# Kernel tuning notes

Measured on AMD Instinct MI355X. Metric: run time of the kernel, lower is better.

## Reference

```python
import jax, jax.numpy as jnp
import numpy as np

TWO_PI = 2.0 * np.pi
EPS = 1e-6

def collect_neighbors(h, edge_idx):
    # h: (B, L, D), edge_idx: (B, L, K) -> (B, L, K, D)
    B, L, K = edge_idx.shape
    D = h.shape[-1]
    flat = jnp.take_along_axis(h, edge_idx.reshape(B, L * K)[..., None], axis=1)
    return flat.reshape(B, L, K, D)

def normalize(v):
    return v / (jnp.linalg.norm(v, axis=-1, keepdims=True) + EPS)

def frames_inverse(X, C):
    # Gram-Schmidt backbone frames: R (B,L,3,3) columns [e1,e2,e3], t = CA
    N, CA, Cc = X[..., 0, :], X[..., 1, :], X[..., 2, :]
    e1 = normalize(N - CA)
    u2 = normalize(Cc - CA)
    e2 = normalize(u2 - jnp.sum(u2 * e1, axis=-1, keepdims=True) * e1)
    e3 = jnp.cross(e1, e2)
    R = jnp.stack([e1, e2, e3], axis=-1)  # (B,L,3,3)
    mask = (C > 0).astype(X.dtype)[..., None]  # (B,L,1)
    t = mask * CA
    R = mask[..., None] * R
    return R, t

def fourier(x, W):
    # x: (..., d_in), W: (d_in, dim_embedding//2)
    h = TWO_PI * jnp.einsum('...d,de->...e', x, W)
    return jnp.concatenate([jnp.cos(h), jnp.sin(h)], axis=-1)

def setup_inputs() -> dict:
    key = jax.random.key(0)
    k1, k2, k3, k4 = jax.random.split(key, 4)
    B, L, K, A = 2, 4096, 32, 4
    half = 128  # dim_embedding // 2
    X = jax.random.normal(k1, (B, L, A, 3), dtype=jnp.float32)
    edge_idx = jax.random.randint(k2, (B, L, K), 0, L)
    C = jnp.ones((B, L), dtype=jnp.int64)
    W_vec = jax.random.normal(k3, (3, half), dtype=jnp.float32)
    W_dist = jax.random.normal(k4, (64, half), dtype=jnp.float32)
    return {"X": X, "edge_idx": edge_idx, "C": C, "W_vec": W_vec, "W_dist": W_dist}

def reference(X, edge_idx, C, W_vec, W_dist):
    B, L, K = edge_idx.shape
    A = X.shape[2]
    # --- Edge2grids: concat i and neighbor-j 1mer coordinates ---
    X_flat = X.reshape(B, L, A * 3)
    X_j = collect_neighbors(X_flat, edge_idx)                      # (B,L,K,A*3)
    X_i = jnp.broadcast_to(X_flat[:, :, None, :], X_j.shape)
    X_ij = jnp.concatenate([X_i, X_j], axis=-1).reshape(B, L, K, 2 * A, 3)
    # --- pairwise distances among the 2A atoms -> (B,L,K,(2A)^2) ---
    dX = X_ij[..., :, None, :] - X_ij[..., None, :, :]
    D_ij = jnp.sqrt(jnp.sum(dX * dX, axis=-1) + EPS)
    D_ij = D_ij.reshape(B, L, K, (2 * A) * (2 * A))                # (B,L,K,64)
    # --- rigid frames + inner-transform composition ---
    R_i, t_i = frames_inverse(X, C)                                # (B,L,3,3), (B,L,3)
    R_j = collect_neighbors(R_i.reshape(B, L, 9), edge_idx).reshape(B, L, K, 3, 3)
    t_j = collect_neighbors(t_i, edge_idx)                         # (B,L,K,3)
    # R_ji = R_i^T R_j ; t_ji = R_i^T (t_j - t_i)
    t_ji = jnp.einsum('blmn,blkm->blkn', R_i, t_j - t_i[:, :, None, :])
    # --- random Fourier features ---
    edge_h = fourier(t_ji, W_vec) + fourier(D_ij, W_dist)          # (B,L,K,256)
    return edge_h
```

## Files before the change

kernel.cpp:

```cpp
#include <hip/hip_runtime.h>


namespace {

constexpr int Bb   = 2;
constexpr int Ll   = 4096;
constexpr int Kk   = 32;
constexpr int HALF = 128;
constexpr float FEPS = 1e-6f;

__device__ __forceinline__ float bcast(float x, int srclane) {
    return __int_as_float(__builtin_amdgcn_readlane(__float_as_int(x), srclane));
}

__global__ __launch_bounds__(128) void edge_rff(
    const float* __restrict__ X,
    const int*   __restrict__ edge_idx,
    const float* __restrict__ Wv,
    const float* __restrict__ Wd,
    float* __restrict__ out)
{
    const int bl   = blockIdx.x;
    const int b    = bl >> 12;
    const int e    = threadIdx.x;
    const int lane = threadIdx.x & 63;

    float w[22];
#pragma unroll
    for (int p = 0; p < 4; ++p)
#pragma unroll
        for (int q = 0; q < 4; ++q)
            w[p*4+q] = Wd[(p*8 + (q+4))*HALF + e] + Wd[((q+4)*8 + p)*HALF + e];

    constexpr int PJ[6] = {0,0,0,1,1,2};
    constexpr int QJ[6] = {1,2,3,2,3,3};
#pragma unroll
    for (int t = 0; t < 6; ++t)
        w[16+t] = Wd[((PJ[t]+4)*8 + (QJ[t]+4))*HALF + e]
                + Wd[((QJ[t]+4)*8 + (PJ[t]+4))*HALF + e];

    float wii[6];
#pragma unroll
    for (int t = 0; t < 6; ++t)
        wii[t] = Wd[(PJ[t]*8 + QJ[t])*HALF + e] + Wd[(QJ[t]*8 + PJ[t])*HALF + e];

    float wdiag = 0.0f;
#pragma unroll
    for (int p = 0; p < 8; ++p) wdiag += Wd[(p*8 + p)*HALF + e];

    const float wv0 = Wv[e], wv1 = Wv[HALF + e], wv2 = Wv[2*HALF + e];

    const float* Xi = X + (size_t)bl * 12;
    const float ai[4][3] = {
        {Xi[0], Xi[1], Xi[2]},
        {Xi[3], Xi[4], Xi[5]},
        {Xi[6], Xi[7], Xi[8]},
        {Xi[9], Xi[10], Xi[11]}
    };

    float cdot = 1.0e-3f * wdiag;
#pragma unroll
    for (int t = 0; t < 6; ++t) {
        const float dx = ai[PJ[t]][0] - ai[QJ[t]][0];
        const float dy = ai[PJ[t]][1] - ai[QJ[t]][1];
        const float dz = ai[PJ[t]][2] - ai[QJ[t]][2];
        cdot = fmaf(sqrtf(fmaf(dx,dx,fmaf(dy,dy,fmaf(dz,dz,FEPS)))), wii[t], cdot);
    }

    const float CAx = ai[1][0], CAy = ai[1][1], CAz = ai[1][2];
    const float v1x = ai[0][0]-CAx, v1y = ai[0][1]-CAy, v1z = ai[0][2]-CAz;
    const float inv1 = 1.0f/(sqrtf(v1x*v1x+v1y*v1y+v1z*v1z)+FEPS);
    const float e1x=v1x*inv1, e1y=v1y*inv1, e1z=v1z*inv1;
    const float v2x = ai[2][0]-CAx, v2y = ai[2][1]-CAy, v2z = ai[2][2]-CAz;
    const float inv2 = 1.0f/(sqrtf(v2x*v2x+v2y*v2y+v2z*v2z)+FEPS);
    const float u2x=v2x*inv2, u2y=v2y*inv2, u2z=v2z*inv2;
    const float dp = u2x*e1x+u2y*e1y+u2z*e1z;
    const float w2x=u2x-dp*e1x, w2y=u2y-dp*e1y, w2z=u2z-dp*e1z;
    const float inv3 = 1.0f/(sqrtf(w2x*w2x+w2y*w2y+w2z*w2z)+FEPS);
    const float e2x=w2x*inv3, e2y=w2y*inv3, e2z=w2z*inv3;
    const float e3x=e1y*e2z-e1z*e2y;
    const float e3y=e1z*e2x-e1x*e2z;
    const float e3z=e1x*e2y-e1y*e2x;

    int pA, pB;
    bool afromj;
    if (lane < 16)      { afromj = false; pA = lane >> 2; pB = lane & 3; }
    else if (lane < 22) { const int tt = lane - 16; afromj = true;
                          pA = (tt < 3) ? 0 : ((tt < 5) ? 1 : 2);
                          pB = (tt < 3) ? (tt + 1) : ((tt < 5) ? (tt - 1) : 3); }
    else                { afromj = false; pA = 0; pB = 0; }
    const float* paConst = Xi + pA * 3;
    const int aoff = pA * 3, boff = pB * 3;

    const int* eidx = edge_idx + (size_t)bl * Kk;
    const int cbase = b * Ll;

    for (int k = 0; k < Kk; ++k) {
        const int j = eidx[k];
        const float* Xj = X + (size_t)(cbase + j) * 12;

        const float* pa = afromj ? (Xj + aoff) : paConst;
        const float* pb = Xj + boff;
        const float dx = pa[0]-pb[0], dy = pa[1]-pb[1], dz = pa[2]-pb[2];
        const float Dlane = sqrtf(fmaf(dx,dx,fmaf(dy,dy,fmaf(dz,dz,FEPS))));

        const float ux = Xj[3]-CAx, uy = Xj[4]-CAy, uz = Xj[5]-CAz;
        const float t0 = e1x*ux + e1y*uy + e1z*uz;
        const float t1 = e2x*ux + e2y*uy + e2z*uz;
        const float t2 = e3x*ux + e3y*uy + e3z*uz;

        float a0 = cdot, a1 = 0.0f, a2 = 0.0f, a3 = 0.0f;
#pragma unroll
        for (int tt = 0; tt < 20; tt += 4) {
            a0 = fmaf(bcast(Dlane, tt+0), w[tt+0], a0);
            a1 = fmaf(bcast(Dlane, tt+1), w[tt+1], a1);
            a2 = fmaf(bcast(Dlane, tt+2), w[tt+2], a2);
            a3 = fmaf(bcast(Dlane, tt+3), w[tt+3], a3);
        }
        a0 = fmaf(bcast(Dlane, 20), w[20], a0);
        a1 = fmaf(bcast(Dlane, 21), w[21], a1);
        const float r2 = (a0 + a1) + (a2 + a3);
        const float r1 = fmaf(t0, wv0, fmaf(t1, wv1, t2 * wv2));

        const float f1 = __builtin_amdgcn_fractf(r1);
        const float f2 = __builtin_amdgcn_fractf(r2);
        const float s1 = __builtin_amdgcn_sinf(f1);
        const float c1 = __builtin_amdgcn_cosf(f1);
        const float s2 = __builtin_amdgcn_sinf(f2);
        const float c2 = __builtin_amdgcn_cosf(f2);

        float* o = out + ((size_t)(bl * Kk + k)) * 256;
        __builtin_nontemporal_store(c1 + c2, o + e);
        __builtin_nontemporal_store(s1 + s2, o + e + 128);
    }
}

}

extern "C" void kernel_launch(void* const* d_in, const int* in_sizes, int n_in,
                              void* d_out, int out_size, void* d_ws, size_t ws_size,
                              hipStream_t stream) {
    const float* X  = (const float*)d_in[0];
    const int*   ei = (const int*)d_in[1];
    const float* Wv = (const float*)d_in[3];
    const float* Wd = (const float*)d_in[4];
    float*       o  = (float*)d_out;

    dim3 grid(Bb * Ll);
    dim3 block(128);
    hipLaunchKernelGGL(edge_rff, grid, block, 0, stream, X, ei, Wv, Wd, o);
}
```

Measured before the change: 326.9 us.

## Precompute per-edge distances and rotated offsets into LDS before the output loop

The kernel now computes all 22 pairwise distances and the three rotated translation components for all 32 neighbours up front. The work is spread across the block's threads and staged in a shared-memory table, followed by one barrier. The output loop then reads these values with vector LDS loads instead of issuing a serial gather and readlane broadcasts per neighbour. This removes the dependent global-load latency and the scalar broadcast chain from each loop iteration, at the cost of LDS traffic, a __syncthreads, and some idle threads in the staging phase.

```diff
diff --git a/kernel.cpp b/kernel.cpp
--- a/kernel.cpp
+++ b/kernel.cpp
@@ -9,10 +9,6 @@
 constexpr int HALF = 128;
 constexpr float FEPS = 1e-6f;
 
-__device__ __forceinline__ float bcast(float x, int srclane) {
-    return __int_as_float(__builtin_amdgcn_readlane(__float_as_int(x), srclane));
-}
-
 __global__ __launch_bounds__(128) void edge_rff(
     const float* __restrict__ X,
     const int*   __restrict__ edge_idx,
@@ -20,10 +16,11 @@
     const float* __restrict__ Wd,
     float* __restrict__ out)
 {
-    const int bl   = blockIdx.x;
-    const int b    = bl >> 12;
-    const int e    = threadIdx.x;
-    const int lane = threadIdx.x & 63;
+    const int bl = blockIdx.x;
+    const int b  = bl >> 12;
+    const int e  = threadIdx.x;
+
+    __shared__ float ed[Kk][28];
 
     float w[22];
 #pragma unroll
@@ -51,27 +48,30 @@
     const float wv0 = Wv[e], wv1 = Wv[HALF + e], wv2 = Wv[2*HALF + e];
 
     const float* Xi = X + (size_t)bl * 12;
-    const float ai[4][3] = {
-        {Xi[0], Xi[1], Xi[2]},
-        {Xi[3], Xi[4], Xi[5]},
-        {Xi[6], Xi[7], Xi[8]},
-        {Xi[9], Xi[10], Xi[11]}
-    };
+    const float Nx  = Xi[0], Ny  = Xi[1], Nz  = Xi[2];
+    const float CAx = Xi[3], CAy = Xi[4], CAz = Xi[5];
+    const float Ccx = Xi[6], Ccy = Xi[7], Ccz = Xi[8];
+    const float Ox  = Xi[9], Oy  = Xi[10], Oz = Xi[11];
 
     float cdot = 1.0e-3f * wdiag;
+    {
+        const float px[4] = {Nx, CAx, Ccx, Ox};
+        const float py[4] = {Ny, CAy, Ccy, Oy};
+        const float pz[4] = {Nz, CAz, Ccz, Oz};
 #pragma unroll
-    for (int t = 0; t < 6; ++t) {
-        const float dx = ai[PJ[t]][0] - ai[QJ[t]][0];
-        const float dy = ai[PJ[t]][1] - ai[QJ[t]][1];
-        const float dz = ai[PJ[t]][2] - ai[QJ[t]][2];
-        cdot = fmaf(sqrtf(fmaf(dx,dx,fmaf(dy,dy,fmaf(dz,dz,FEPS)))), wii[t], cdot);
+        for (int t = 0; t < 6; ++t) {
+            const float dx = px[PJ[t]] - px[QJ[t]];
+            const float dy = py[PJ[t]] - py[QJ[t]];
+            const float dz = pz[PJ[t]] - pz[QJ[t]];
+            cdot = fmaf(sqrtf(fmaf(dx,dx,fmaf(dy,dy,fmaf(dz,dz,FEPS)))),
+                        wii[t], cdot);
+        }
     }
 
-    const float CAx = ai[1][0], CAy = ai[1][1], CAz = ai[1][2];
-    const float v1x = ai[0][0]-CAx, v1y = ai[0][1]-CAy, v1z = ai[0][2]-CAz;
+    const float v1x = Nx-CAx, v1y = Ny-CAy, v1z = Nz-CAz;
     const float inv1 = 1.0f/(sqrtf(v1x*v1x+v1y*v1y+v1z*v1z)+FEPS);
     const float e1x=v1x*inv1, e1y=v1y*inv1, e1z=v1z*inv1;
-    const float v2x = ai[2][0]-CAx, v2y = ai[2][1]-CAy, v2z = ai[2][2]-CAz;
+    const float v2x = Ccx-CAx, v2y = Ccy-CAy, v2z = Ccz-CAz;
     const float inv2 = 1.0f/(sqrtf(v2x*v2x+v2y*v2y+v2z*v2z)+FEPS);
     const float u2x=v2x*inv2, u2y=v2y*inv2, u2z=v2z*inv2;
     const float dp = u2x*e1x+u2y*e1y+u2z*e1z;
@@ -82,45 +82,68 @@
     const float e3y=e1z*e2x-e1x*e2z;
     const float e3z=e1x*e2y-e1y*e2x;
 
-    int pA, pB;
-    bool afromj;
-    if (lane < 16)      { afromj = false; pA = lane >> 2; pB = lane & 3; }
-    else if (lane < 22) { const int tt = lane - 16; afromj = true;
-                          pA = (tt < 3) ? 0 : ((tt < 5) ? 1 : 2);
-                          pB = (tt < 3) ? (tt + 1) : ((tt < 5) ? (tt - 1) : 3); }
-    else                { afromj = false; pA = 0; pB = 0; }
-    const float* paConst = Xi + pA * 3;
-    const int aoff = pA * 3, boff = pB * 3;
+    const int* eidx  = edge_idx + (size_t)bl * Kk;
+    const int  cbase = b * Ll;
 
-    const int* eidx = edge_idx + (size_t)bl * Kk;
-    const int cbase = b * Ll;
-
-    for (int k = 0; k < Kk; ++k) {
-        const int j = eidx[k];
+#pragma unroll
+    for (int i = 0; i < 8; ++i) {
+        const int id   = threadIdx.x + i * 128;
+        const int edge = id >> 5;
+        const int slot = id & 31;
+        if (slot >= 25) continue;
+        const int j = eidx[edge];
         const float* Xj = X + (size_t)(cbase + j) * 12;
 
-        const float* pa = afromj ? (Xj + aoff) : paConst;
-        const float* pb = Xj + boff;
-        const float dx = pa[0]-pb[0], dy = pa[1]-pb[1], dz = pa[2]-pb[2];
-        const float Dlane = sqrtf(fmaf(dx,dx,fmaf(dy,dy,fmaf(dz,dz,FEPS))));
+        float val;
+        if (slot < 22) {
+            const int tt  = (slot >= 16) ? (slot - 16) : 0;
+            const int pja = (0x211000 >> (4*tt)) & 0xF;
+            const int qja = (0x332321 >> (4*tt)) & 0xF;
+            const float* pa = (slot < 16) ? (Xi + (slot >> 2) * 3)
+                                          : (Xj + pja * 3);
+            const float* pb = (slot < 16) ? (Xj + (slot & 3) * 3)
+                                          : (Xj + qja * 3);
+            const float dx = pa[0]-pb[0], dy = pa[1]-pb[1], dz = pa[2]-pb[2];
+            val = sqrtf(fmaf(dx,dx,fmaf(dy,dy,fmaf(dz,dz,FEPS))));
+        } else {
+            const int m = slot - 22;
+            const float ux = Xj[3]-CAx, uy = Xj[4]-CAy, uz = Xj[5]-CAz;
+            const float emx = (m==0) ? e1x : ((m==1) ? e2x : e3x);
+            const float emy = (m==0) ? e1y : ((m==1) ? e2y : e3y);
+            const float emz = (m==0) ? e1z : ((m==1) ? e2z : e3z);
+            val = fmaf(emx, ux, fmaf(emy, uy, emz * uz));
+        }
+        ed[edge][slot] = val;
+    }
 
-        const float ux = Xj[3]-CAx, uy = Xj[4]-CAy, uz = Xj[5]-CAz;
-        const float t0 = e1x*ux + e1y*uy + e1z*uz;
-        const float t1 = e2x*ux + e2y*uy + e2z*uz;
-        const float t2 = e3x*ux + e3y*uy + e3z*uz;
+    __syncthreads();
+
+    float* obase = out + (size_t)bl * (Kk * 256) + e;
+
+#pragma unroll 4
+    for (int k = 0; k < Kk; ++k) {
+        const float4 d0 = *(const float4*)&ed[k][0];
+        const float4 d1 = *(const float4*)&ed[k][4];
+        const float4 d2 = *(const float4*)&ed[k][8];
+        const float4 d3 = *(const float4*)&ed[k][12];
+        const float4 d4 = *(const float4*)&ed[k][16];
+        const float4 d5 = *(const float4*)&ed[k][20];
+        const float  t2v = ed[k][24];
 
         float a0 = cdot, a1 = 0.0f, a2 = 0.0f, a3 = 0.0f;
-#pragma unroll
-        for (int tt = 0; tt < 20; tt += 4) {
-            a0 = fmaf(bcast(Dlane, tt+0), w[tt+0], a0);
-            a1 = fmaf(bcast(Dlane, tt+1), w[tt+1], a1);
-            a2 = fmaf(bcast(Dlane, tt+2), w[tt+2], a2);
-            a3 = fmaf(bcast(Dlane, tt+3), w[tt+3], a3);
-        }
-        a0 = fmaf(bcast(Dlane, 20), w[20], a0);
-        a1 = fmaf(bcast(Dlane, 21), w[21], a1);
+        a0 = fmaf(d0.x, w[0],  a0); a1 = fmaf(d0.y, w[1],  a1);
+        a2 = fmaf(d0.z, w[2],  a2); a3 = fmaf(d0.w, w[3],  a3);
+        a0 = fmaf(d1.x, w[4],  a0); a1 = fmaf(d1.y, w[5],  a1);
+        a2 = fmaf(d1.z, w[6],  a2); a3 = fmaf(d1.w, w[7],  a3);
+        a0 = fmaf(d2.x, w[8],  a0); a1 = fmaf(d2.y, w[9],  a1);
+        a2 = fmaf(d2.z, w[10], a2); a3 = fmaf(d2.w, w[11], a3);
+        a0 = fmaf(d3.x, w[12], a0); a1 = fmaf(d3.y, w[13], a1);
+        a2 = fmaf(d3.z, w[14], a2); a3 = fmaf(d3.w, w[15], a3);
+        a0 = fmaf(d4.x, w[16], a0); a1 = fmaf(d4.y, w[17], a1);
+        a2 = fmaf(d4.z, w[18], a2); a3 = fmaf(d4.w, w[19], a3);
+        a0 = fmaf(d5.x, w[20], a0); a1 = fmaf(d5.y, w[21], a1);
         const float r2 = (a0 + a1) + (a2 + a3);
-        const float r1 = fmaf(t0, wv0, fmaf(t1, wv1, t2 * wv2));
+        const float r1 = fmaf(d5.z, wv0, fmaf(d5.w, wv1, t2v * wv2));
 
         const float f1 = __builtin_amdgcn_fractf(r1);
         const float f2 = __builtin_amdgcn_fractf(r2);
@@ -129,9 +152,8 @@
         const float s2 = __builtin_amdgcn_sinf(f2);
         const float c2 = __builtin_amdgcn_cosf(f2);
 
-        float* o = out + ((size_t)(bl * Kk + k)) * 256;
-        __builtin_nontemporal_store(c1 + c2, o + e);
-        __builtin_nontemporal_store(s1 + s2, o + e + 128);
+        __builtin_nontemporal_store(c1 + c2, obase + (size_t)k * 256);
+        __builtin_nontemporal_store(s1 + s2, obase + (size_t)k * 256 + 128);
     }
 }
 
```

Result: faster. 302.1 us (-7.6%).
